# Performance work log

Measured on AMD Instinct MI355X. Metric: run time of the kernel, lower is better.

The kernel has to match this reference:

```python
import jax, jax.numpy as jnp
import numpy as np

B, L, E, H, D, DFF = 2, 2048, 1024, 16, 64, 4096
SCALE = D ** 0.5


def rmsnorm(x):
    # NOTE: original uses mean(x*x)**0.5 with no eps and no learned scale
    rms = jnp.sqrt(jnp.mean(x * x, axis=-1, keepdims=True))
    return x / rms


def alibi_matrix():
    i = jnp.arange(L)
    dists = -jnp.abs(i[None, :] - i[:, None]).astype(jnp.float32)  # [L, L]
    slopes = 2.0 ** (-jnp.linspace(1.0, 8.0, H))                   # [H]
    alibi = slopes[:, None, None] * dists                          # [H, L, L]
    causal = jnp.tril(jnp.ones((L, L), dtype=bool))
    return jnp.where(causal[None], alibi, -jnp.inf)[None]          # [1, H, L, L]


def setup_inputs() -> dict:
    key = jax.random.key(0)
    ks = jax.random.split(key, 16)
    s = 0.02
    return {
        "X": jax.random.normal(ks[0], (B, L, E), jnp.float32),
        "encoder_out": jax.random.normal(ks[1], (B, L, E), jnp.float32),
        # self-attention params
        "Wqkv": jax.random.normal(ks[2], (E, 3 * H * D), jnp.float32) * s,
        "bqkv": jnp.zeros((3 * H * D,), jnp.float32),
        "Wo_sa": jax.random.normal(ks[3], (H * D, E), jnp.float32) * s,
        "bo_sa": jnp.zeros((E,), jnp.float32),
        # cross-attention params (computed by torch module but its forward returns X, so unused)
        "Wq": jax.random.normal(ks[4], (E, H * D), jnp.float32) * s,
        "bq": jnp.zeros((H * D,), jnp.float32),
        "Wkv": jax.random.normal(ks[5], (E, 2 * H * D), jnp.float32) * s,
        "bkv": jnp.zeros((2 * H * D,), jnp.float32),
        "Wo_ca": jax.random.normal(ks[6], (H * D, E), jnp.float32) * s,
        "bo_ca": jnp.zeros((E,), jnp.float32),
        # GLU FFN params (bias=False)
        "Ww": jax.random.normal(ks[7], (E, DFF), jnp.float32) * s,
        "Wv": jax.random.normal(ks[8], (E, DFF), jnp.float32) * s,
        "Wout": jax.random.normal(ks[9], (DFF, E), jnp.float32) * s,
    }


def reference(X, encoder_out, Wqkv, bqkv, Wo_sa, bo_sa, Wq, bq, Wkv, bkv,
              Wo_ca, bo_ca, Ww, Wv, Wout):
    alibi = alibi_matrix()

    # ---- self-attention (pre-norm + residual) ----
    h = rmsnorm(X)
    qkv = (h @ Wqkv + bqkv).reshape(B, L, H, 3, D)
    Q, K, V = qkv[..., 0, :], qkv[..., 1, :], qkv[..., 2, :]      # [B, L, H, D]
    scores = jnp.einsum('blhd,bmhd->bhlm', Q, K) / SCALE + alibi  # [B, H, L, L]
    attn = jax.nn.softmax(scores, axis=-1)
    ctx = jnp.einsum('bhlm,bmhd->blhd', attn, V).reshape(B, L, H * D)
    X = X + ctx @ Wo_sa + bo_sa

    # ---- cross-attention stage ----
    # Faithful to source: CrossAttention.forward returns its input X (the
    # normalized tensor) rather than the attention output, so this block is
    # X + rmsnorm(X). Cross-attn params never affect the output.
    X = X + rmsnorm(X)

    # ---- GLU FFN (pre-norm + residual), exact (erf) GELU as in torch F.gelu ----
    h = rmsnorm(X)
    ff = jax.nn.gelu(h @ Ww, approximate=False) * (h @ Wv)
    X = X + ff @ Wout
    return X
```

## Files before the change

### kernel.cpp

```cpp
#include <hip/hip_runtime.h>

#define B_SZ 2
#define L_SEQ 2048
#define E_DIM 1024
#define NH 16
#define DH 64
#define DFF_DIM 4096
#define ROWS (B_SZ * L_SEQ)

typedef __attribute__((ext_vector_type(8))) short short8;
typedef __attribute__((ext_vector_type(4))) float f32x4;

__device__ __forceinline__ short f2bf(float f) {
  unsigned u = __builtin_bit_cast(unsigned, f);
  u = (u + 0x7FFFu + ((u >> 16) & 1u)) >> 16;
  return (short)u;
}
__device__ __forceinline__ float bf2f(short s) {
  unsigned u = ((unsigned)(unsigned short)s) << 16;
  return __builtin_bit_cast(float, u);
}

__device__ __forceinline__ void async_copy16(const void* g, void* l) {
  __builtin_amdgcn_global_load_lds(
      (const __attribute__((address_space(1))) void*)g,
      (__attribute__((address_space(3))) void*)l, 16, 0, 0);
}

__device__ __forceinline__ float block_sum256(float v) {
  __shared__ float sbuf[4];
#pragma unroll
  for (int off = 32; off > 0; off >>= 1) v += __shfl_xor(v, off, 64);
  int lane = threadIdx.x & 63, w = threadIdx.x >> 6;
  if (lane == 0) sbuf[w] = v;
  __syncthreads();
  return sbuf[0] + sbuf[1] + sbuf[2] + sbuf[3];
}

__global__ __launch_bounds__(256) void prep_all(
    const float* __restrict__ Wqkv, const float* __restrict__ Wo,
    const float* __restrict__ Ww, const float* __restrict__ Wv,
    const float* __restrict__ Wout, const float* __restrict__ X,
    short* __restrict__ WqkvT, short* __restrict__ WoT,
    short* __restrict__ Bcat, short* __restrict__ WoutT,
    short* __restrict__ H) {
  __shared__ float tile[32][33];
  int b = blockIdx.x;
  if (b < 16384) {
    const float* W;
    short* Wt;
    int K, N, poff, bx, by;
    if (b < 3072) {
      W = Wqkv; Wt = WqkvT; K = 1024; N = 3072; poff = -1;
      bx = b % 96; by = b / 96;
    } else if (b < 4096) {
      int c = b - 3072;
      W = Wo; Wt = WoT; K = 1024; N = 1024; poff = -1;
      bx = c & 31; by = c >> 5;
    } else if (b < 8192) {
      int c = b - 4096;
      W = Ww; Wt = Bcat; K = 1024; N = 4096; poff = 0;
      bx = c & 127; by = c >> 7;
    } else if (b < 12288) {
      int c = b - 8192;
      W = Wv; Wt = Bcat; K = 1024; N = 4096; poff = 64;
      bx = c & 127; by = c >> 7;
    } else {
      int c = b - 12288;
      W = Wout; Wt = WoutT; K = 4096; N = 1024; poff = -1;
      bx = c & 31; by = c >> 5;
    }
    int n0 = bx * 32, k0 = by * 32;
    int tx = threadIdx.x & 31, ty = threadIdx.x >> 5;
#pragma unroll
    for (int i = 0; i < 4; i++)
      tile[ty + 8 * i][tx] = W[(size_t)(k0 + ty + 8 * i) * N + n0 + tx];
    __syncthreads();
#pragma unroll
    for (int i = 0; i < 4; i++) {
      int n = n0 + ty + 8 * i;
      int orow = (poff < 0) ? n : ((n >> 6) * 128 + (n & 63) + poff);
      Wt[(size_t)orow * K + k0 + tx] = f2bf(tile[tx][ty + 8 * i]);
    }
  } else {
    size_t row = b - 16384;
    float4 v = ((const float4*)(X + row * E_DIM))[threadIdx.x];
    float ss = v.x * v.x + v.y * v.y + v.z * v.z + v.w * v.w;
    ss = block_sum256(ss);
    float inv = rsqrtf(ss * (1.0f / E_DIM));
    short* h = H + row * E_DIM + (size_t)threadIdx.x * 4;
    h[0] = f2bf(v.x * inv);
    h[1] = f2bf(v.y * inv);
    h[2] = f2bf(v.z * inv);
    h[3] = f2bf(v.w * inv);
  }
}

__global__ __launch_bounds__(256) void resid_rms_fused(
    const float* __restrict__ X, const float* __restrict__ P0,
    const float* __restrict__ P1, const float* __restrict__ bias,
    float* __restrict__ Xout, short* __restrict__ H) {
  size_t row = blockIdx.x;
  int t = threadIdx.x;
  float4 v = ((const float4*)(X + row * E_DIM))[t];
  float4 a = ((const float4*)(P0 + row * E_DIM))[t];
  float4 b = ((const float4*)(P1 + row * E_DIM))[t];
  float4 c = ((const float4*)bias)[t];
  v.x += a.x + b.x + c.x;
  v.y += a.y + b.y + c.y;
  v.z += a.z + b.z + c.z;
  v.w += a.w + b.w + c.w;
  float ss = v.x * v.x + v.y * v.y + v.z * v.z + v.w * v.w;
  ss = block_sum256(ss);
  float inv = rsqrtf(ss * (1.0f / E_DIM));
  float4 o;
  o.x = v.x * (1.0f + inv);
  o.y = v.y * (1.0f + inv);
  o.z = v.z * (1.0f + inv);
  o.w = v.w * (1.0f + inv);
  ((float4*)(Xout + row * E_DIM))[t] = o;
  short* h = H + row * E_DIM + (size_t)t * 4;
  h[0] = f2bf(v.x * inv);
  h[1] = f2bf(v.y * inv);
  h[2] = f2bf(v.z * inv);
  h[3] = f2bf(v.w * inv);
}

__global__ __launch_bounds__(256) void add2_k(const float* __restrict__ X2,
                                              const float* __restrict__ P0,
                                              const float* __restrict__ P1,
                                              float* __restrict__ out) {
  size_t i = (size_t)blockIdx.x * 256 + threadIdx.x;
  float4 v = ((const float4*)X2)[i];
  float4 a = ((const float4*)P0)[i];
  float4 b = ((const float4*)P1)[i];
  v.x += a.x + b.x;
  v.y += a.y + b.y;
  v.z += a.z + b.z;
  v.w += a.w + b.w;
  ((float4*)out)[i] = v;
}

__global__ __launch_bounds__(256, 2) void gemm_bt(
    const short* __restrict__ A, const short* __restrict__ Bt,
    const float* __restrict__ bias, const float* __restrict__ res,
    void* __restrict__ out, int M, int N, int K, int epi, int ksplit) {
  __shared__ short smem[128 * 32 * 4];
  short* As0 = smem;
  short* Bs0 = smem + 4096;
  short* As1 = smem + 8192;
  short* Bs1 = smem + 12288;
  int t = threadIdx.x;
  int lane = t & 63;
  int quad = lane >> 4, l16 = lane & 15;
  int wave = t >> 6;
  int wr = wave >> 1, wc = wave & 1;
  int m0 = blockIdx.y * 128, n0 = blockIdx.x * 128;
  int klen = K / ksplit;
  int kstart = blockIdx.z * klen;

  f32x4 acc[4][4];
#pragma unroll
  for (int i = 0; i < 4; i++)
#pragma unroll
    for (int j = 0; j < 4; j++) acc[i][j] = (f32x4){0.f, 0.f, 0.f, 0.f};

  for (int k0 = kstart; k0 < kstart + klen; k0 += 64) {
    __syncthreads();
#pragma unroll
    for (int p = 0; p < 2; p++) {
      int s = p * 256 + t;
      int mm = s >> 2, kk = (s & 3) * 8;
      const short* ag = A + (size_t)(m0 + mm) * K + k0 + kk;
      const short* bg = Bt + (size_t)(n0 + mm) * K + k0 + kk;
      async_copy16(ag, As0 + (size_t)s * 8);
      async_copy16(bg, Bs0 + (size_t)s * 8);
      async_copy16(ag + 32, As1 + (size_t)s * 8);
      async_copy16(bg + 32, Bs1 + (size_t)s * 8);
    }
    __syncthreads();
#pragma unroll
    for (int half = 0; half < 2; half++) {
      const short* As = half ? As1 : As0;
      const short* Bs = half ? Bs1 : Bs0;
      short8 af[4], bfv[4];
#pragma unroll
      for (int i = 0; i < 4; i++) {
        af[i] = *(const short8*)&As[(wr * 64 + i * 16 + l16) * 32 + quad * 8];
        bfv[i] = *(const short8*)&Bs[(wc * 64 + i * 16 + l16) * 32 + quad * 8];
      }
#pragma unroll
      for (int mi = 0; mi < 4; mi++)
#pragma unroll
        for (int ni = 0; ni < 4; ni++)
          acc[mi][ni] = __builtin_amdgcn_mfma_f32_16x16x32_bf16(
              af[mi], bfv[ni], acc[mi][ni], 0, 0, 0);
    }
  }

  if (epi == 5) {
    __syncthreads();
    short* xbuf = smem;
    if (wc == 0) {
#pragma unroll
      for (int mi = 0; mi < 4; mi++)
#pragma unroll
        for (int ni = 0; ni < 4; ni++)
#pragma unroll
          for (int r = 0; r < 4; r++) {
            int rowl = wr * 64 + mi * 16 + quad * 4 + r;
            float v = acc[mi][ni][r];
            float g = 0.5f * v * (1.0f + erff(v * 0.70710678118654752f));
            xbuf[rowl * 68 + ni * 16 + l16] = f2bf(g);
          }
    }
    __syncthreads();
    if (wc == 1) {
      short* FF = (short*)out;
#pragma unroll
      for (int mi = 0; mi < 4; mi++)
#pragma unroll
        for (int ni = 0; ni < 4; ni++)
#pragma unroll
          for (int r = 0; r < 4; r++) {
            int rowl = wr * 64 + mi * 16 + quad * 4 + r;
            int coll = ni * 16 + l16;
            float w = bf2f(xbuf[rowl * 68 + coll]);
            FF[(size_t)(m0 + rowl) * DFF_DIM + blockIdx.x * 64 + coll] =
                f2bf(w * acc[mi][ni][r]);
          }
    }
    return;
  }

#pragma unroll
  for (int mi = 0; mi < 4; mi++) {
#pragma unroll
    for (int ni = 0; ni < 4; ni++) {
      int col = n0 + wc * 64 + ni * 16 + l16;
      float bv = bias ? bias[col] : 0.0f;
#pragma unroll
      for (int r = 0; r < 4; r++) {
        int row = m0 + wr * 64 + mi * 16 + quad * 4 + r;
        size_t idx = (size_t)row * N + col;
        float v = acc[mi][ni][r] + bv;
        if (epi == 0) {
          ((short*)out)[idx] = f2bf(v);
        } else if (epi == 3) {
          ((float*)out)[idx] = v + res[idx];
        } else {
          float* po = (float*)out + (size_t)blockIdx.z * ((size_t)M * N);
          po[idx] = v;
        }
      }
    }
  }
}

__global__ __launch_bounds__(256) void kv_prep(const short* __restrict__ qkv,
                                               short* __restrict__ Kh,
                                               short* __restrict__ VTh) {
  int lt = blockIdx.x, bh = blockIdx.y;
  int b = bh >> 4, h = bh & 15;
  __shared__ short vtile[64 * 72];
  int t = threadIdx.x;
  int r = t >> 3, c = (t & 7) * 8;
  const short* base =
      qkv + (size_t)(b * L_SEQ + lt * 64) * (3 * NH * DH) + h * (3 * DH);
#pragma unroll
  for (int p = 0; p < 2; p++) {
    int row = r + p * 32;
    short8 kv = *(const short8*)(base + (size_t)row * (3 * NH * DH) + DH + c);
    *(short8*)(Kh + ((size_t)bh * L_SEQ + lt * 64 + row) * DH + c) = kv;
    short8 vv =
        *(const short8*)(base + (size_t)row * (3 * NH * DH) + 2 * DH + c);
    *(short8*)&vtile[row * 72 + c] = vv;
  }
  __syncthreads();
#pragma unroll
  for (int p = 0; p < 2; p++) {
    int d = r + p * 32;
    short8 o;
#pragma unroll
    for (int u = 0; u < 8; u++) o[u] = vtile[(c + u) * 72 + d];
    *(short8*)(VTh + ((size_t)bh * DH + d) * L_SEQ + lt * 64 + c) = o;
  }
}

__global__ __launch_bounds__(256) void attn_k(const short* __restrict__ qkv,
                                              const short* __restrict__ Kh,
                                              const short* __restrict__ VTh,
                                              short* __restrict__ ctx) {
  int qt = (gridDim.x - 1) - blockIdx.x;
  int bh = blockIdx.y;
  int b = bh >> 4, h = bh & 15;
  int t = threadIdx.x;
  int wave = t >> 6, lane = t & 63;
  int quad = lane >> 4, l16 = lane & 15;

  __shared__ short kt[64 * 72];
  __shared__ short vt[64 * 72];
  __shared__ short pb[4 * 16 * 70];

  const float slope = exp2f(-(1.0f + (7.0f / 15.0f) * (float)h));
  const size_t rowstride = 3 * NH * DH;
  const short* qbase = qkv + (size_t)(b * L_SEQ) * rowstride + h * (3 * DH);
  int iw = qt * 64 + wave * 16;

  short8 qf[2];
  {
    const short* qp = qbase + (size_t)(iw + l16) * rowstride + quad * 8;
    qf[0] = *(const short8*)(qp);
    qf[1] = *(const short8*)(qp + 32);
  }

  f32x4 o[4];
#pragma unroll
  for (int i = 0; i < 4; i++) o[i] = (f32x4){0.f, 0.f, 0.f, 0.f};
  float rs[4] = {0.f, 0.f, 0.f, 0.f};
  float crow[4];
  int irow[4];
#pragma unroll
  for (int r = 0; r < 4; r++) {
    irow[r] = iw + quad * 4 + r;
    crow[r] = -slope * (float)irow[r] - 8.0f;
  }

  int sr = t >> 3, sc = (t & 7) * 8;
  const short* kg = Kh + (size_t)bh * L_SEQ * DH;
  const short* vg = VTh + (size_t)bh * DH * L_SEQ;
  short8 kreg[2], vreg[2];
  auto loadKV = [&](int j0) {
    kreg[0] = *(const short8*)(kg + (size_t)(j0 + sr) * DH + sc);
    kreg[1] = *(const short8*)(kg + (size_t)(j0 + sr + 32) * DH + sc);
    vreg[0] = *(const short8*)(vg + (size_t)sr * L_SEQ + j0 + sc);
    vreg[1] = *(const short8*)(vg + (size_t)(sr + 32) * L_SEQ + j0 + sc);
  };
  loadKV(0);

  short* pw = &pb[wave * 16 * 70];
  int ntile = qt + 1;
  for (int tix = 0; tix < ntile; ++tix) {
    int j0 = tix * 64;
    __syncthreads();
    *(short8*)&kt[sr * 72 + sc] = kreg[0];
    *(short8*)&kt[(sr + 32) * 72 + sc] = kreg[1];
    *(short8*)&vt[sr * 72 + sc] = vreg[0];
    *(short8*)&vt[(sr + 32) * 72 + sc] = vreg[1];
    __syncthreads();
    if (tix + 1 < ntile) loadKV(j0 + 64);

    f32x4 s[4];
#pragma unroll
    for (int nt = 0; nt < 4; nt++) {
      f32x4 a = (f32x4){0.f, 0.f, 0.f, 0.f};
#pragma unroll
      for (int ks = 0; ks < 2; ks++) {
        short8 bf =
            *(const short8*)&kt[(nt * 16 + l16) * 72 + ks * 32 + quad * 8];
        a = __builtin_amdgcn_mfma_f32_16x16x32_bf16(qf[ks], bf, a, 0, 0, 0);
      }
      s[nt] = a;
    }
    bool diag = (tix == ntile - 1);
#pragma unroll
    for (int nt = 0; nt < 4; nt++) {
      int j = j0 + nt * 16 + l16;
      float jb = slope * (float)j;
#pragma unroll
      for (int r = 0; r < 4; r++) {
        float v = __builtin_fmaf(s[nt][r], 0.125f, jb + crow[r]);
        if (diag && j > irow[r]) v = -1e30f;
        float p = __expf(v);
        rs[r] += p;
        pw[(quad * 4 + r) * 70 + nt * 16 + l16] = f2bf(p);
      }
    }
    short8 pf[2];
    pf[0] = *(const short8*)&pw[l16 * 70 + quad * 8];
    pf[1] = *(const short8*)&pw[l16 * 70 + 32 + quad * 8];
#pragma unroll
    for (int nt = 0; nt < 4; nt++) {
#pragma unroll
      for (int ks = 0; ks < 2; ks++) {
        short8 bv =
            *(const short8*)&vt[(nt * 16 + l16) * 72 + ks * 32 + quad * 8];
        o[nt] = __builtin_amdgcn_mfma_f32_16x16x32_bf16(pf[ks], bv, o[nt], 0,
                                                        0, 0);
      }
    }
  }
#pragma unroll
  for (int r = 0; r < 4; r++) {
#pragma unroll
    for (int off = 1; off < 16; off <<= 1) rs[r] += __shfl_xor(rs[r], off, 64);
    float inv = 1.0f / rs[r];
    short* dst = ctx + (size_t)(b * L_SEQ + irow[r]) * (NH * DH) + h * DH;
#pragma unroll
    for (int nt = 0; nt < 4; nt++) dst[nt * 16 + l16] = f2bf(o[nt][r] * inv);
  }
}

extern "C" void kernel_launch(void* const* d_in, const int* in_sizes, int n_in,
                              void* d_out, int out_size, void* d_ws,
                              size_t ws_size, hipStream_t stream) {
  const float* X = (const float*)d_in[0];
  const float* Wqkv = (const float*)d_in[2];
  const float* bqkv = (const float*)d_in[3];
  const float* Wo_sa = (const float*)d_in[4];
  const float* bo_sa = (const float*)d_in[5];
  const float* Ww = (const float*)d_in[12];
  const float* Wv = (const float*)d_in[13];
  const float* Wout = (const float*)d_in[14];

  char* ws = (char*)d_ws;
  auto take = [&](size_t bytes) {
    char* p = ws;
    ws += (bytes + 255) & ~(size_t)255;
    return p;
  };
  short* WqkvT = (short*)take((size_t)3 * NH * DH * E_DIM * 2);
  short* WoT = (short*)take((size_t)E_DIM * E_DIM * 2);
  short* Bcat = (short*)take((size_t)2 * DFF_DIM * E_DIM * 2);
  short* WoutT = (short*)take((size_t)E_DIM * DFF_DIM * 2);
  short* Hbuf = (short*)take((size_t)ROWS * E_DIM * 2);
  short* QKV = (short*)take((size_t)ROWS * 3 * NH * DH * 2);
  short* CTX = (short*)take((size_t)ROWS * NH * DH * 2);
  float* X1 = (float*)take((size_t)ROWS * E_DIM * 4);
  short* KVb = (short*)take((size_t)2 * B_SZ * NH * L_SEQ * DH * 2);
  short* FF = (short*)take((size_t)ROWS * DFF_DIM * 2);
  short* Kh = KVb;
  short* VTh = KVb + (size_t)B_SZ * NH * L_SEQ * DH;
  float* Pwo = (float*)FF;
  float* Pwout = (float*)QKV;
  (void)ws_size;
  (void)in_sizes;
  (void)n_in;
  (void)out_size;

  dim3 blk(256);
  prep_all<<<16384 + ROWS, blk, 0, stream>>>(Wqkv, Wo_sa, Ww, Wv, Wout, X,
                                             WqkvT, WoT, Bcat, WoutT, Hbuf);
  gemm_bt<<<dim3(3072 / 128, ROWS / 128), blk, 0, stream>>>(
      Hbuf, WqkvT, bqkv, nullptr, QKV, ROWS, 3072, 1024, 0, 1);
  kv_prep<<<dim3(L_SEQ / 64, B_SZ * NH), blk, 0, stream>>>(QKV, Kh, VTh);
  attn_k<<<dim3(L_SEQ / 64, B_SZ * NH), blk, 0, stream>>>(QKV, Kh, VTh, CTX);
  gemm_bt<<<dim3(1024 / 128, ROWS / 128, 2), blk, 0, stream>>>(
      CTX, WoT, nullptr, nullptr, Pwo, ROWS, 1024, 1024, 4, 2);
  resid_rms_fused<<<ROWS, blk, 0, stream>>>(
      X, Pwo, Pwo + (size_t)ROWS * E_DIM, bo_sa, X1, Hbuf);
  gemm_bt<<<dim3(2 * DFF_DIM / 128, ROWS / 128), blk, 0, stream>>>(
      Hbuf, Bcat, nullptr, nullptr, FF, ROWS, 2 * DFF_DIM, 1024, 5, 1);
  gemm_bt<<<dim3(1024 / 128, ROWS / 128, 2), blk, 0, stream>>>(
      FF, WoutT, nullptr, nullptr, Pwout, ROWS, 1024, 4096, 4, 2);
  add2_k<<<ROWS * E_DIM / (256 * 4), blk, 0, stream>>>(
      X1, Pwout, Pwout + (size_t)ROWS * E_DIM, (float*)d_out);
}
```

Baseline: 470.7 us.

## Split causal attention KV range into chunks with separate merge kernel

Causal attention blocks are split along the key dimension into chunks of up to 8 tiles. Each query tile now gets 1 to 4 blocks, 80 per head instead of 32, which evens out work across blocks and raises block count. Partial unnormalised outputs and row sums are written in fp32 to a workspace reused from X1. A new merge kernel sums the chunks and normalises. This is possible because the softmax uses a fixed offset rather than a running max. The cost is the extra fp32 partial traffic and one more kernel launch.

```diff
diff --git a/kernel.cpp b/kernel.cpp
--- a/kernel.cpp
+++ b/kernel.cpp
@@ -7,6 +7,7 @@
 #define DH 64
 #define DFF_DIM 4096
 #define ROWS (B_SZ * L_SEQ)
+#define NCID 80
 
 typedef __attribute__((ext_vector_type(8))) short short8;
 typedef __attribute__((ext_vector_type(4))) float f32x4;
@@ -290,10 +291,24 @@
 __global__ __launch_bounds__(256) void attn_k(const short* __restrict__ qkv,
                                               const short* __restrict__ Kh,
                                               const short* __restrict__ VTh,
-                                              short* __restrict__ ctx) {
-  int qt = (gridDim.x - 1) - blockIdx.x;
+                                              float* __restrict__ OP,
+                                              float* __restrict__ RS) {
+  int cid = blockIdx.x;
   int bh = blockIdx.y;
   int b = bh >> 4, h = bh & 15;
+  int qt, ch;
+  if (cid < 8) {
+    qt = cid; ch = 0;
+  } else if (cid < 24) {
+    qt = 8 + ((cid - 8) >> 1); ch = (cid - 8) & 1;
+  } else if (cid < 48) {
+    qt = 16 + (cid - 24) / 3; ch = (cid - 24) % 3;
+  } else {
+    qt = 24 + ((cid - 48) >> 2); ch = (cid - 48) & 3;
+  }
+  int t0 = ch * 8;
+  int tend = min(t0 + 8, qt + 1);
+
   int t = threadIdx.x;
   int wave = t >> 6, lane = t & 63;
   int quad = lane >> 4, l16 = lane & 15;
@@ -336,11 +351,10 @@
     vreg[0] = *(const short8*)(vg + (size_t)sr * L_SEQ + j0 + sc);
     vreg[1] = *(const short8*)(vg + (size_t)(sr + 32) * L_SEQ + j0 + sc);
   };
-  loadKV(0);
+  loadKV(t0 * 64);
 
   short* pw = &pb[wave * 16 * 70];
-  int ntile = qt + 1;
-  for (int tix = 0; tix < ntile; ++tix) {
+  for (int tix = t0; tix < tend; ++tix) {
     int j0 = tix * 64;
     __syncthreads();
     *(short8*)&kt[sr * 72 + sc] = kreg[0];
@@ -348,7 +362,7 @@
     *(short8*)&vt[sr * 72 + sc] = vreg[0];
     *(short8*)&vt[(sr + 32) * 72 + sc] = vreg[1];
     __syncthreads();
-    if (tix + 1 < ntile) loadKV(j0 + 64);
+    if (tix + 1 < tend) loadKV(j0 + 64);
 
     f32x4 s[4];
 #pragma unroll
@@ -362,7 +376,7 @@
       }
       s[nt] = a;
     }
-    bool diag = (tix == ntile - 1);
+    bool diag = (tix == qt);
 #pragma unroll
     for (int nt = 0; nt < 4; nt++) {
       int j = j0 + nt * 16 + l16;
@@ -390,15 +404,56 @@
       }
     }
   }
+  float* op = OP + ((size_t)bh * NCID + cid) * 64 * 64;
+  float* rsp = RS + ((size_t)bh * NCID + cid) * 64;
 #pragma unroll
   for (int r = 0; r < 4; r++) {
 #pragma unroll
     for (int off = 1; off < 16; off <<= 1) rs[r] += __shfl_xor(rs[r], off, 64);
-    float inv = 1.0f / rs[r];
-    short* dst = ctx + (size_t)(b * L_SEQ + irow[r]) * (NH * DH) + h * DH;
-#pragma unroll
-    for (int nt = 0; nt < 4; nt++) dst[nt * 16 + l16] = f2bf(o[nt][r] * inv);
-  }
+    int rowl = wave * 16 + quad * 4 + r;
+#pragma unroll
+    for (int nt = 0; nt < 4; nt++) op[rowl * 64 + nt * 16 + l16] = o[nt][r];
+    if (l16 == 0) rsp[rowl] = rs[r];
+  }
+}
+
+__global__ __launch_bounds__(256) void attn_merge(const float* __restrict__ OP,
+                                                  const float* __restrict__ RS,
+                                                  short* __restrict__ ctx) {
+  int row = blockIdx.x;
+  int b = row >> 11, i = row & 2047;
+  int qt = i >> 6, rowin = i & 63;
+  int base, nch;
+  if (qt < 8) {
+    base = qt; nch = 1;
+  } else if (qt < 16) {
+    base = 8 + 2 * (qt - 8); nch = 2;
+  } else if (qt < 24) {
+    base = 24 + 3 * (qt - 16); nch = 3;
+  } else {
+    base = 48 + 4 * (qt - 24); nch = 4;
+  }
+  int t = threadIdx.x;
+  int col = t * 4;
+  int h = col >> 6;
+  int bh = b * NH + h;
+  float4 o = {0.f, 0.f, 0.f, 0.f};
+  float l = 0.f;
+  for (int s = 0; s < nch; s++) {
+    size_t cb = ((size_t)bh * NCID + base + s) * 64 + rowin;
+    float4 v = *(const float4*)&OP[cb * 64 + (col & 63)];
+    o.x += v.x;
+    o.y += v.y;
+    o.z += v.z;
+    o.w += v.w;
+    l += RS[cb];
+  }
+  float inv = 1.0f / l;
+  short* dst = ctx + (size_t)row * (NH * DH) + col;
+  dst[0] = f2bf(o.x * inv);
+  dst[1] = f2bf(o.y * inv);
+  dst[2] = f2bf(o.z * inv);
+  dst[3] = f2bf(o.w * inv);
 }
 
 extern "C" void kernel_launch(void* const* d_in, const int* in_sizes, int n_in,
@@ -426,11 +481,13 @@
   short* Hbuf = (short*)take((size_t)ROWS * E_DIM * 2);
   short* QKV = (short*)take((size_t)ROWS * 3 * NH * DH * 2);
   short* CTX = (short*)take((size_t)ROWS * NH * DH * 2);
+  short* KVb = (short*)take((size_t)2 * B_SZ * NH * L_SEQ * DH * 2);
   float* X1 = (float*)take((size_t)ROWS * E_DIM * 4);
-  short* KVb = (short*)take((size_t)2 * B_SZ * NH * L_SEQ * DH * 2);
   short* FF = (short*)take((size_t)ROWS * DFF_DIM * 2);
   short* Kh = KVb;
   short* VTh = KVb + (size_t)B_SZ * NH * L_SEQ * DH;
+  float* OP = (float*)X1;
+  float* RS = OP + (size_t)B_SZ * NH * NCID * 64 * 64;
   float* Pwo = (float*)FF;
   float* Pwout = (float*)QKV;
   (void)ws_size;
@@ -444,7 +501,8 @@
   gemm_bt<<<dim3(3072 / 128, ROWS / 128), blk, 0, stream>>>(
       Hbuf, WqkvT, bqkv, nullptr, QKV, ROWS, 3072, 1024, 0, 1);
   kv_prep<<<dim3(L_SEQ / 64, B_SZ * NH), blk, 0, stream>>>(QKV, Kh, VTh);
-  attn_k<<<dim3(L_SEQ / 64, B_SZ * NH), blk, 0, stream>>>(QKV, Kh, VTh, CTX);
+  attn_k<<<dim3(NCID, B_SZ * NH), blk, 0, stream>>>(QKV, Kh, VTh, OP, RS);
+  attn_merge<<<ROWS, blk, 0, stream>>>(OP, RS, CTX);
   gemm_bt<<<dim3(1024 / 128, ROWS / 128, 2), blk, 0, stream>>>(
       CTX, WoT, nullptr, nullptr, Pwo, ROWS, 1024, 1024, 4, 2);
   resid_rms_fused<<<ROWS, blk, 0, stream>>>(
```

Result: faster. 441.8 us (-6.2%).
